# Kernel optimization log

Measured on AMD Instinct MI355X. Metric: run time of the kernel, lower is better.

The kernel has to match this reference:

```python
import jax, jax.numpy as jnp
import numpy as np

ACT_BITS = 8
W_BITS = 8
BN_EPS = 1e-5


def _round_ste(x):
    # straight-through round (HAWQ-style ste_round)
    return x + jax.lax.stop_gradient(jnp.round(x) - x)


def _quant_sym(x, bits):
    # symmetric per-tensor fake quantization; scale treated as constant (EMA min/max in original)
    n = float(2 ** (bits - 1) - 1)
    s = jax.lax.stop_gradient(jnp.maximum(jnp.max(jnp.abs(x)) / n, 1e-8))
    xq = jnp.clip(_round_ste(x / s), -n - 1.0, n) * s
    return xq, s


def _conv(x, w, stride, pad):
    return jax.lax.conv_general_dilated(
        x, w, (stride, stride), [(pad, pad), (pad, pad)],
        dimension_numbers=("NCHW", "OIHW", "NCHW"))


def _quant_bn(x, gamma, beta, mean, var):
    # fold BN into a per-channel scale+bias; quantize the folded scale like a weight
    ws = gamma * jax.lax.rsqrt(var + BN_EPS)          # [C]
    wq, ws_scale = _quant_sym(ws, W_BITS)
    b = beta - mean * wq                               # [C]
    return x * wq[None, :, None, None] + b[None, :, None, None], ws_scale


def setup_inputs() -> dict:
    key = jax.random.key(0)
    ks = jax.random.split(key, 16)
    d = {}
    d["x"] = jax.random.normal(ks[0], (32, 128, 56, 56), jnp.float32)
    d["w1"] = jax.random.normal(ks[1], (256, 128, 3, 3), jnp.float32) * 0.05
    d["w2"] = jax.random.normal(ks[2], (256, 256, 3, 3), jnp.float32) * 0.05
    d["w_id"] = jax.random.normal(ks[3], (256, 128, 1, 1), jnp.float32) * 0.05
    for i, pfx in enumerate(["bn1", "bn2", "id"]):
        k4 = jax.random.split(ks[4 + i], 4)
        d[pfx + "_gamma"] = jax.random.uniform(k4[0], (256,), jnp.float32) + 0.5
        d[pfx + "_beta"] = jax.random.normal(k4[1], (256,), jnp.float32) * 0.1
        d[pfx + "_mean"] = jax.random.normal(k4[2], (256,), jnp.float32) * 0.1
        d[pfx + "_var"] = jax.random.uniform(k4[3], (256,), jnp.float32) + 0.5
    return d


def reference(x, w1, w2, w_id,
              bn1_gamma, bn1_beta, bn1_mean, bn1_var,
              bn2_gamma, bn2_beta, bn2_mean, bn2_var,
              id_gamma, id_beta, id_mean, id_var):
    # quant_act on block input
    xq, act_s = _quant_sym(x, ACT_BITS)

    # identity branch: 1x1 stride-2 quantized conv -> quant_act -> folded quant bn
    w_id_q, _ = _quant_sym(w_id, W_BITS)
    identity = _conv(xq, w_id_q, 2, 0)
    identity, _ = _quant_sym(identity, ACT_BITS)
    identity, _ = _quant_bn(identity, id_gamma, id_beta, id_mean, id_var)

    # main branch conv1 (3x3 stride 2) -> act quant -> bn -> relu -> act quant
    w1_q, _ = _quant_sym(w1, W_BITS)
    h = _conv(xq, w1_q, 2, 1)
    h, _ = _quant_sym(h, ACT_BITS)
    h, _ = _quant_bn(h, bn1_gamma, bn1_beta, bn1_mean, bn1_var)
    h = jax.nn.relu(h)
    h, _ = _quant_sym(h, ACT_BITS)

    # conv2 (3x3 stride 1) -> act quant -> bn
    w2_q, _ = _quant_sym(w2, W_BITS)
    h = _conv(h, w2_q, 1, 1)
    h, _ = _quant_sym(h, ACT_BITS)
    h, _ = _quant_bn(h, bn2_gamma, bn2_beta, bn2_mean, bn2_var)

    # residual add -> int32 requant -> relu
    h = h + identity
    h, out_s = _quant_sym(h, ACT_BITS)
    h = jax.nn.relu(h)
    return h, out_s
```

## Files before the change

kernel.cpp:

```cpp
#include <hip/hip_runtime.h>
#include <limits.h>

#define THREADS 256

typedef int vi4 __attribute__((ext_vector_type(4)));

__device__ __forceinline__ float clamp8f(float q) { return fminf(fmaxf(q, -128.0f), 127.0f); }
__device__ __forceinline__ float sc_from_bits(unsigned b) {
  return fmaxf(__uint_as_float(b) / 127.0f, 1e-8f);
}
__device__ __forceinline__ signed char q8(float v, float s) {
  return (signed char)(int)clamp8f(rintf(v / s));
}


__global__ __launch_bounds__(THREADS) void k_init(int* IS, int* maxv, int* minv) {
  int t = threadIdx.x;
  if (t < 64) IS[t] = 0;
  maxv[t] = INT_MIN;
  minv[t] = INT_MAX;
}

__global__ __launch_bounds__(THREADS) void k_amax(const float4* __restrict__ p, int n4,
                                                  unsigned* __restrict__ slot) {
  const int tid = threadIdx.x;
  const int stride = gridDim.x * THREADS;
  float m = 0.0f;
  int i = blockIdx.x * THREADS + tid;
  for (; i + 3 * stride < n4; i += 4 * stride) {
    float4 v0 = p[i];
    float4 v1 = p[i + stride];
    float4 v2 = p[i + 2 * stride];
    float4 v3 = p[i + 3 * stride];
    float m0 = fmaxf(fmaxf(fabsf(v0.x), fabsf(v0.y)), fmaxf(fabsf(v0.z), fabsf(v0.w)));
    float m1 = fmaxf(fmaxf(fabsf(v1.x), fabsf(v1.y)), fmaxf(fabsf(v1.z), fabsf(v1.w)));
    float m2 = fmaxf(fmaxf(fabsf(v2.x), fabsf(v2.y)), fmaxf(fabsf(v2.z), fabsf(v2.w)));
    float m3 = fmaxf(fmaxf(fabsf(v3.x), fabsf(v3.y)), fmaxf(fabsf(v3.z), fabsf(v3.w)));
    m = fmaxf(m, fmaxf(fmaxf(m0, m1), fmaxf(m2, m3)));
  }
  for (; i < n4; i += stride) {
    float4 v = p[i];
    m = fmaxf(m, fmaxf(fmaxf(fabsf(v.x), fabsf(v.y)), fmaxf(fabsf(v.z), fabsf(v.w))));
  }
#pragma unroll
  for (int k = 32; k >= 1; k >>= 1) m = fmaxf(m, __shfl_xor(m, k));
  __shared__ float wred[4];
  if ((tid & 63) == 0) wred[tid >> 6] = m;
  __syncthreads();
  if (tid == 0) {
    m = fmaxf(fmaxf(wred[0], wred[1]), fmaxf(wred[2], wred[3]));
    atomicMax(slot, __float_as_uint(m));
  }
}

__global__ __launch_bounds__(THREADS) void k_bnfold(const float* __restrict__ gamma,
                                                    const float* __restrict__ beta,
                                                    const float* __restrict__ mean,
                                                    const float* __restrict__ var,
                                                    float* __restrict__ wq, float* __restrict__ bb) {
  __shared__ float red[THREADS];
  int c = threadIdx.x;
  float ws = gamma[c] * (1.0f / sqrtf(var[c] + 1e-5f));
  red[c] = fabsf(ws);
  __syncthreads();
  for (int s = THREADS / 2; s > 0; s >>= 1) {
    if (c < s) red[c] = fmaxf(red[c], red[c + s]);
    __syncthreads();
  }
  float sws = fmaxf(red[0] / 127.0f, 1e-8f);
  float q = clamp8f(rintf(ws / sws)) * sws;
  wq[c] = q;
  bb[c] = beta[c] - mean[c] * q;
}

__global__ __launch_bounds__(THREADS) void k_qx(const float* __restrict__ x, int* __restrict__ X8,
                                                const unsigned* __restrict__ ISu) {
  __shared__ signed char tile[56 * 132];
  float s = sc_from_bits(ISu[0]);
  int b = blockIdx.x;
  int h = b % 56, n = b / 56;
  int t = threadIdx.x;
  const float* xp = x + ((n * 128) * 56 + h) * 56;
#pragma unroll
  for (int k = 0; k < 28; ++k) {
    int i = t + k * 256;
    int w = i % 56, c = i / 56;
    tile[w * 132 + c] = q8(xp[c * 3136 + w], s);
  }
  __syncthreads();
  int* op = X8 + (n * 56 + h) * 56 * 32;
#pragma unroll
  for (int k = 0; k < 7; ++k) {
    int i = t + k * 256;
    int w = i >> 5, c4 = (i & 31) * 4;
    const signed char* tp = tile + w * 132 + c4;
    op[i] = (int)(unsigned char)tp[0] | ((int)(unsigned char)tp[1] << 8) |
            ((int)(unsigned char)tp[2] << 16) | ((int)(unsigned char)tp[3] << 24);
  }
}

__global__ __launch_bounds__(THREADS) void k_qw2m(const float* __restrict__ w, vi4* __restrict__ wm,
                                                  const unsigned* __restrict__ ISu) {
  int t = blockIdx.x * THREADS + threadIdx.x;
  float s = sc_from_bits(ISu[2]);
  int lane = t & 63;
  int cotile = (t >> 6) & 15;
  int ks = t >> 10;
  int tap = ks >> 2, kc = ks & 3;
  int kh = tap / 3, kw = tap % 3;
  int co = cotile * 16 + (lane & 15);
  int ci0 = kc * 64 + (lane >> 4) * 16;
  const float* src = w + (co * 256 + ci0) * 9 + kh * 3 + kw;
  int r[4];
#pragma unroll
  for (int q = 0; q < 4; ++q) {
    unsigned b0 = (unsigned char)q8(src[(q * 4 + 0) * 9], s);
    unsigned b1 = (unsigned char)q8(src[(q * 4 + 1) * 9], s);
    unsigned b2 = (unsigned char)q8(src[(q * 4 + 2) * 9], s);
    unsigned b3 = (unsigned char)q8(src[(q * 4 + 3) * 9], s);
    r[q] = (int)(b0 | (b1 << 8) | (b2 << 16) | (b3 << 24));
  }
  vi4 v = {r[0], r[1], r[2], r[3]};
  wm[t] = v;
}

__global__ __launch_bounds__(THREADS) void k_qw1m(const float* __restrict__ w, vi4* __restrict__ wm,
                                                  const unsigned* __restrict__ ISu) {
  int t = blockIdx.x * THREADS + threadIdx.x;
  float s = sc_from_bits(ISu[1]);
  int lane = t & 63;
  int cotile = (t >> 6) & 15;
  int ks = t >> 10;
  int tap = ks >> 1, kc = ks & 1;
  int kh = tap / 3, kw = tap % 3;
  int co = cotile * 16 + (lane & 15);
  int ci0 = kc * 64 + (lane >> 4) * 16;
  const float* src = w + (co * 128 + ci0) * 9 + kh * 3 + kw;
  int r[4];
#pragma unroll
  for (int q = 0; q < 4; ++q) {
    unsigned b0 = (unsigned char)q8(src[(q * 4 + 0) * 9], s);
    unsigned b1 = (unsigned char)q8(src[(q * 4 + 1) * 9], s);
    unsigned b2 = (unsigned char)q8(src[(q * 4 + 2) * 9], s);
    unsigned b3 = (unsigned char)q8(src[(q * 4 + 3) * 9], s);
    r[q] = (int)(b0 | (b1 << 8) | (b2 << 16) | (b3 << 24));
  }
  vi4 v = {r[0], r[1], r[2], r[3]};
  wm[t] = v;
}

__global__ __launch_bounds__(THREADS) void k_qwidm(const float* __restrict__ w,
                                                   vi4* __restrict__ wm,
                                                   const unsigned* __restrict__ ISu) {
  int t = blockIdx.x * THREADS + threadIdx.x;
  float s = sc_from_bits(ISu[3]);
  int lane = t & 63;
  int cotile = (t >> 6) & 15;
  int ks = t >> 10;
  int co = cotile * 16 + (lane & 15);
  int ci0 = ks * 64 + (lane >> 4) * 16;
  const float* src = w + co * 128 + ci0;
  int r[4];
#pragma unroll
  for (int q = 0; q < 4; ++q) {
    unsigned b0 = (unsigned char)q8(src[q * 4 + 0], s);
    unsigned b1 = (unsigned char)q8(src[q * 4 + 1], s);
    unsigned b2 = (unsigned char)q8(src[q * 4 + 2], s);
    unsigned b3 = (unsigned char)q8(src[q * 4 + 3], s);
    r[q] = (int)(b0 | (b1 << 8) | (b2 << 16) | (b3 << 24));
  }
  vi4 v = {r[0], r[1], r[2], r[3]};
  wm[t] = v;
}

#define MFMA_I8(a, b, c) __builtin_amdgcn_mfma_i32_16x16x64_i8(a, b, c, 0, 0, 0)

__global__ __launch_bounds__(THREADS, 2) void k_conv1(const int* __restrict__ X8,
                                                      const vi4* __restrict__ W1m,
                                                      const vi4* __restrict__ Widm,
                                                      int* __restrict__ H1, int* __restrict__ IDI,
                                                      int* __restrict__ maxS,
                                                      int* __restrict__ minS,
                                                      int* __restrict__ maxabs_id) {
  __shared__ __align__(16) int lds[5 * 58 * 36];
  __shared__ int sMax[2][128], sMin[2][128], redA[4];
  const int tid = threadIdx.x;
  const int bx = blockIdx.x;
  const int n = bx / 28, rr = bx % 28;
  const int hp = rr >> 1, nh = rr & 1;
  const int ho0 = hp * 2;

  for (int r = 0; r < 5; ++r) {
    int h = 2 * ho0 - 1 + r;
    int* dst = lds + r * 58 * 36;
    if (h >= 0 && h < 56) {
      const int* src = X8 + (n * 56 + h) * 56 * 32;
      for (int i = tid; i < 56 * 32; i += THREADS) {
        int col = i >> 5, c = i & 31;
        dst[(col + 1) * 36 + c] = src[i];
      }
      if (tid < 32) dst[tid] = 0;
      else if (tid >= 128 && tid < 160) dst[57 * 36 + (tid - 128)] = 0;
    } else {
      for (int i = tid; i < 58 * 36; i += THREADS) dst[i] = 0;
    }
  }
  __syncthreads();

  const int lane = tid & 63, wv = tid >> 6;
  const int mw = wv & 1, nw = wv >> 1;
  const int lm = lane & 15, quad = lane >> 4;
  const int woc0 = lm, woc1 = (16 + lm) > 27 ? 27 : (16 + lm);
  const int choff = quad * 4;
  const int ho = ho0 + mw;
  const int obase = ((n * 28 + ho) * 28) * 256;
  const int ctbase = nh * 8 + nw * 4;

  vi4 zero = {0, 0, 0, 0};
  vi4 acc[2][4];
  vi4 bcur[4], bnext[4];
  vi4 a0c, a1c, a0n, a1n;

#pragma unroll
  for (int mt = 0; mt < 2; ++mt)
#pragma unroll
    for (int ct = 0; ct < 4; ++ct) acc[mt][ct] = zero;
  const vi4* wibase = Widm + ctbase * 64 + lane;
  {
    const int ro = (2 * mw + 1) * 58;
#pragma unroll
    for (int kc = 0; kc < 2; ++kc) {
      vi4 a0 = *(const vi4*)(lds + (ro + 2 * woc0 + 1) * 36 + kc * 16 + choff);
      vi4 a1 = *(const vi4*)(lds + (ro + 2 * woc1 + 1) * 36 + kc * 16 + choff);
#pragma unroll
      for (int ct = 0; ct < 4; ++ct) {
        vi4 b = wibase[kc * 1024 + ct * 64];
        acc[0][ct] = MFMA_I8(a0, b, acc[0][ct]);
        acc[1][ct] = MFMA_I8(a1, b, acc[1][ct]);
      }
    }
  }
  int am = 0;
#pragma unroll
  for (int ct = 0; ct < 4; ++ct) {
    const int co = (ctbase + ct) * 16 + lm;
#pragma unroll
    for (int mt = 0; mt < 2; ++mt)
#pragma unroll
      for (int r = 0; r < 4; ++r) {
        int wo = mt * 16 + quad * 4 + r;
        if (wo < 28) {
          int v = acc[mt][ct][r];
          IDI[obase + wo * 256 + co] = v;
          am = max(am, v < 0 ? -v : v);
        }
      }
  }
#pragma unroll
  for (int k = 32; k >= 1; k >>= 1) am = max(am, __shfl_xor(am, k));
  if (lane == 0) redA[wv] = am;

#pragma unroll
  for (int mt = 0; mt < 2; ++mt)
#pragma unroll
    for (int ct = 0; ct < 4; ++ct) acc[mt][ct] = zero;
  const vi4* wbase = W1m + ctbase * 64 + lane;
#pragma unroll
  for (int ct = 0; ct < 4; ++ct) bcur[ct] = wbase[ct * 64];
  {
    const int ro = (2 * mw) * 58;
    a0c = *(const vi4*)(lds + (ro + 2 * woc0) * 36 + choff);
    a1c = *(const vi4*)(lds + (ro + 2 * woc1) * 36 + choff);
  }
#pragma unroll 1
  for (int ks = 0; ks < 18; ++ks) {
    int ksn = ks + 1;
    if (ksn < 18) {
      int khn = (ksn >= 6) + (ksn >= 12);
      int t2 = ksn - khn * 6;
      int kwn = t2 >> 1, kcn = t2 & 1;
#pragma unroll
      for (int ct = 0; ct < 4; ++ct) bnext[ct] = wbase[ksn * 1024 + ct * 64];
      int ro = (2 * mw + khn) * 58;
      a0n = *(const vi4*)(lds + (ro + 2 * woc0 + kwn) * 36 + kcn * 16 + choff);
      a1n = *(const vi4*)(lds + (ro + 2 * woc1 + kwn) * 36 + kcn * 16 + choff);
    }
#pragma unroll
    for (int ct = 0; ct < 4; ++ct) {
      acc[0][ct] = MFMA_I8(a0c, bcur[ct], acc[0][ct]);
      acc[1][ct] = MFMA_I8(a1c, bcur[ct], acc[1][ct]);
    }
    a0c = a0n;
    a1c = a1n;
#pragma unroll
    for (int ct = 0; ct < 4; ++ct) bcur[ct] = bnext[ct];
  }

#pragma unroll
  for (int ct = 0; ct < 4; ++ct) {
    const int co = (ctbase + ct) * 16 + lm;
    int vmax = INT_MIN, vmin = INT_MAX;
#pragma unroll
    for (int mt = 0; mt < 2; ++mt)
#pragma unroll
      for (int r = 0; r < 4; ++r) {
        int wo = mt * 16 + quad * 4 + r;
        if (wo < 28) {
          int v = acc[mt][ct][r];
          H1[obase + wo * 256 + co] = v;
          vmax = max(vmax, v);
          vmin = min(vmin, v);
        }
      }
    vmax = max(vmax, __shfl_xor(vmax, 16));
    vmax = max(vmax, __shfl_xor(vmax, 32));
    vmin = min(vmin, __shfl_xor(vmin, 16));
    vmin = min(vmin, __shfl_xor(vmin, 32));
    if (lane < 16) {
      sMax[mw][nw * 64 + ct * 16 + lane] = vmax;
      sMin[mw][nw * 64 + ct * 16 + lane] = vmin;
    }
  }
  __syncthreads();
  if (tid < 128) {
    int row = n * 14 + hp;
    maxS[row * 256 + nh * 128 + tid] = max(sMax[0][tid], sMax[1][tid]);
    minS[row * 256 + nh * 128 + tid] = min(sMin[0][tid], sMin[1][tid]);
  }
  if (tid == 0) {
    int a = max(max(redA[0], redA[1]), max(redA[2], redA[3]));
    atomicMax(maxabs_id, a);
  }
}

__global__ __launch_bounds__(THREADS) void k_red(const int* __restrict__ maxS,
                                                 const int* __restrict__ minS,
                                                 int* __restrict__ maxv, int* __restrict__ minv) {
  int c = threadIdx.x, b = blockIdx.x;
  int vx = INT_MIN, vn = INT_MAX;
#pragma unroll
  for (int r = 0; r < 14; ++r) {
    int row = b * 14 + r;
    vx = max(vx, maxS[row * 256 + c]);
    vn = min(vn, minS[row * 256 + c]);
  }
  atomicMax(&maxv[c], vx);
  atomicMin(&minv[c], vn);
}

__global__ __launch_bounds__(THREADS) void k_s1(int* __restrict__ IS, float* __restrict__ SC,
                                                const int* __restrict__ maxv,
                                                const int* __restrict__ minv,
                                                const float* __restrict__ wq1,
                                                const float* __restrict__ b1) {
  __shared__ int ri[THREADS];
  __shared__ float rf[THREADS];
  int c = threadIdx.x;
  int vmax = maxv[c], vmin = minv[c];
  int a1 = vmax < 0 ? -vmax : vmax;
  int a0 = vmin < 0 ? -vmin : vmin;
  ri[c] = max(a1, a0);
  __syncthreads();
  for (int s = THREADS / 2; s > 0; s >>= 1) {
    if (c < s) ri[c] = max(ri[c], ri[c + s]);
    __syncthreads();
  }
  int mh1 = ri[0];
  const unsigned* ISu = (const unsigned*)IS;
  float sx = sc_from_bits(ISu[0]);
  float sw1 = sc_from_bits(ISu[1]);
  float sxw = sx * sw1;
  float s_h1 = fmaxf(sxw * (float)mh1 / 127.0f, 1e-8f);
  float wq = wq1[c], bbc = b1[c];
  float q1 = clamp8f(rintf((float)vmax * sxw / s_h1));
  float q0 = clamp8f(rintf((float)vmin * sxw / s_h1));
  float hv1 = q1 * s_h1, hv0 = q0 * s_h1;
  float y1 = fmaxf(hv1 * wq + bbc, 0.0f);
  float y0 = fmaxf(hv0 * wq + bbc, 0.0f);
  rf[c] = fmaxf(y1, y0);
  __syncthreads();
  for (int s = THREADS / 2; s > 0; s >>= 1) {
    if (c < s) rf[c] = fmaxf(rf[c], rf[c + s]);
    __syncthreads();
  }
  if (c == 0) {
    IS[4] = mh1;
    SC[7] = rf[0];
    SC[8] = s_h1;
    SC[9] = fmaxf(rf[0] / 127.0f, 1e-8f);
    float swid = sc_from_bits(ISu[3]);
    SC[10] = fmaxf(sx * swid * (float)IS[5] / 127.0f, 1e-8f);
  }
}

__device__ __forceinline__ signed char qact(int v, float sxw, float s_h1, float s_y2, float wq,
                                            float bb) {
  float hf = (float)v * sxw;
  float q = clamp8f(rintf(hf / s_h1));
  float hv = q * s_h1;
  float y = fmaxf(hv * wq + bb, 0.0f);
  float a = fminf(fmaxf(rintf(y / s_y2), -128.0f), 127.0f);
  return (signed char)(int)a;
}

__global__ __launch_bounds__(THREADS) void k_qh1(const int4* __restrict__ H1,
                                                 char4* __restrict__ A2,
                                                 const float* __restrict__ SC,
                                                 const float* __restrict__ wq1,
                                                 const float* __restrict__ b1) {
  int t = blockIdx.x * THREADS + threadIdx.x;
  const unsigned* ISu = (const unsigned*)SC;
  float sx = sc_from_bits(ISu[0]);
  float sw1 = sc_from_bits(ISu[1]);
  float sxw = sx * sw1;
  float s_h1 = SC[8];
  float s_y2 = SC[9];
  int4 v = H1[t];
  int c0 = (t * 4) & 255;
  char4 r;
  r.x = qact(v.x, sxw, s_h1, s_y2, wq1[c0], b1[c0]);
  r.y = qact(v.y, sxw, s_h1, s_y2, wq1[c0 + 1], b1[c0 + 1]);
  r.z = qact(v.z, sxw, s_h1, s_y2, wq1[c0 + 2], b1[c0 + 2]);
  r.w = qact(v.w, sxw, s_h1, s_y2, wq1[c0 + 3], b1[c0 + 3]);
  A2[t] = r;
}

__global__ __launch_bounds__(THREADS, 2) void k_conv2(const int* __restrict__ A2,
                                                      const vi4* __restrict__ W2m,
                                                      int* __restrict__ H2,
                                                      int* __restrict__ maxabs_h2) {
  __shared__ __align__(16) int lds[4 * 30 * 68];
  __shared__ int redA[4];
  const int tid = threadIdx.x;
  const int bx = blockIdx.x;
  const int n = bx / 28, rr = bx % 28;
  const int hp = rr >> 1, nh = rr & 1;
  const int ho0 = hp * 2;

  for (int r = 0; r < 4; ++r) {
    int h = ho0 - 1 + r;
    int* dst = lds + r * 30 * 68;
    if (h >= 0 && h < 28) {
      const int* src = A2 + (n * 28 + h) * 28 * 64;
      for (int i = tid; i < 28 * 64; i += THREADS) {
        int col = i >> 6, c = i & 63;
        dst[(col + 1) * 68 + c] = src[i];
      }
      if (tid < 64) dst[tid] = 0;
      else if (tid >= 128 && tid < 192) dst[29 * 68 + (tid - 128)] = 0;
    } else {
      for (int i = tid; i < 30 * 68; i += THREADS) dst[i] = 0;
    }
  }
  __syncthreads();

  const int lane = tid & 63, wv = tid >> 6;
  const int mw = wv & 1, nw = wv >> 1;
  const int lm = lane & 15, quad = lane >> 4;
  const int woc0 = lm, woc1 = (16 + lm) > 27 ? 27 : (16 + lm);
  const int choff = quad * 4;
  const int ho = ho0 + mw;
  const int ctbase = nh * 8 + nw * 4;

  vi4 zero = {0, 0, 0, 0};
  vi4 acc[2][4];
#pragma unroll
  for (int mt = 0; mt < 2; ++mt)
#pragma unroll
    for (int ct = 0; ct < 4; ++ct) acc[mt][ct] = zero;

  const vi4* wbase = W2m + ctbase * 64 + lane;
  vi4 bcur[4], bnext[4];
  vi4 a0c, a1c, a0n, a1n;
#pragma unroll
  for (int ct = 0; ct < 4; ++ct) bcur[ct] = wbase[ct * 64];
  {
    const int ro = mw * 30;
    a0c = *(const vi4*)(lds + (ro + woc0) * 68 + choff);
    a1c = *(const vi4*)(lds + (ro + woc1) * 68 + choff);
  }
#pragma unroll 1
  for (int ks = 0; ks < 36; ++ks) {
    int ksn = ks + 1;
    if (ksn < 36) {
      int khn = (ksn >= 12) + (ksn >= 24);
      int t2 = ksn - khn * 12;
      int kwn = t2 >> 2, kcn = t2 & 3;
#pragma unroll
      for (int ct = 0; ct < 4; ++ct) bnext[ct] = wbase[ksn * 1024 + ct * 64];
      int ro = (mw + khn) * 30;
      a0n = *(const vi4*)(lds + (ro + woc0 + kwn) * 68 + kcn * 16 + choff);
      a1n = *(const vi4*)(lds + (ro + woc1 + kwn) * 68 + kcn * 16 + choff);
    }
#pragma unroll
    for (int ct = 0; ct < 4; ++ct) {
      acc[0][ct] = MFMA_I8(a0c, bcur[ct], acc[0][ct]);
      acc[1][ct] = MFMA_I8(a1c, bcur[ct], acc[1][ct]);
    }
    a0c = a0n;
    a1c = a1n;
#pragma unroll
    for (int ct = 0; ct < 4; ++ct) bcur[ct] = bnext[ct];
  }

  const int obase = ((n * 28 + ho) * 28) * 256;
  int am = 0;
#pragma unroll
  for (int ct = 0; ct < 4; ++ct) {
    const int co = (ctbase + ct) * 16 + lm;
#pragma unroll
    for (int mt = 0; mt < 2; ++mt)
#pragma unroll
      for (int r = 0; r < 4; ++r) {
        int wo = mt * 16 + quad * 4 + r;
        if (wo < 28) {
          int v = acc[mt][ct][r];
          H2[obase + wo * 256 + co] = v;
          am = max(am, v < 0 ? -v : v);
        }
      }
  }
#pragma unroll
  for (int k = 32; k >= 1; k >>= 1) am = max(am, __shfl_xor(am, k));
  if (lane == 0) redA[wv] = am;
  __syncthreads();
  if (tid == 0) {
    int a = max(max(redA[0], redA[1]), max(redA[2], redA[3]));
    atomicMax(maxabs_h2, a);
  }
}

struct SumParams {
  float sxw2, s_h2, sxwid, s_idq;
};
__device__ __forceinline__ float sum_val(int v2, int vi, const SumParams& P, float wq2c, float b2c,
                                         float wqidc, float bidc) {
  float q2 = clamp8f(rintf((float)v2 * P.sxw2 / P.s_h2));
  float z = (q2 * P.s_h2) * wq2c + b2c;
  float qi = clamp8f(rintf((float)vi * P.sxwid / P.s_idq));
  float zi = (qi * P.s_idq) * wqidc + bidc;
  return z + zi;
}
__device__ __forceinline__ SumParams make_params(const float* SC, const int* IS) {
  const unsigned* ISu = (const unsigned*)IS;
  SumParams P;
  float sx = sc_from_bits(ISu[0]);
  float sw2 = sc_from_bits(ISu[2]);
  float swid = sc_from_bits(ISu[3]);
  float s_y2 = SC[9];
  P.s_idq = SC[10];
  P.sxw2 = s_y2 * sw2;
  P.s_h2 = fmaxf(P.sxw2 * (float)IS[6] / 127.0f, 1e-8f);
  P.sxwid = sx * swid;
  return P;
}

__global__ __launch_bounds__(THREADS) void k_absmax2(const int4* __restrict__ H2,
                                                     const int4* __restrict__ IDI,
                                                     const float* __restrict__ SC,
                                                     const int* __restrict__ IS,
                                                     const float* __restrict__ wq2,
                                                     const float* __restrict__ b2,
                                                     const float* __restrict__ wqid,
                                                     const float* __restrict__ bidp,
                                                     unsigned* __restrict__ slot) {
  __shared__ float pw2[256], pb2[256], pwi[256], pbi[256];
  int tid = threadIdx.x;
  pw2[tid] = wq2[tid];
  pb2[tid] = b2[tid];
  pwi[tid] = wqid[tid];
  pbi[tid] = bidp[tid];
  __syncthreads();
  SumParams P = make_params(SC, IS);
  const int n4 = 1605632;
  const int stride = gridDim.x * THREADS;
  float m = 0.0f;
  for (int i = blockIdx.x * THREADS + tid; i < n4; i += stride) {
    int4 v2 = H2[i];
    int4 vi = IDI[i];
    int c0 = (i * 4) & 255;
    m = fmaxf(m, fabsf(sum_val(v2.x, vi.x, P, pw2[c0], pb2[c0], pwi[c0], pbi[c0])));
    m = fmaxf(m, fabsf(sum_val(v2.y, vi.y, P, pw2[c0 + 1], pb2[c0 + 1], pwi[c0 + 1], pbi[c0 + 1])));
    m = fmaxf(m, fabsf(sum_val(v2.z, vi.z, P, pw2[c0 + 2], pb2[c0 + 2], pwi[c0 + 2], pbi[c0 + 2])));
    m = fmaxf(m, fabsf(sum_val(v2.w, vi.w, P, pw2[c0 + 3], pb2[c0 + 3], pwi[c0 + 3], pbi[c0 + 3])));
  }
#pragma unroll
  for (int k = 32; k >= 1; k >>= 1) m = fmaxf(m, __shfl_xor(m, k));
  __shared__ float wred[4];
  if ((tid & 63) == 0) wred[tid >> 6] = m;
  __syncthreads();
  if (tid == 0) {
    m = fmaxf(fmaxf(wred[0], wred[1]), fmaxf(wred[2], wred[3]));
    atomicMax(slot, __float_as_uint(m));
  }
}

__global__ __launch_bounds__(THREADS) void k_out(const int* __restrict__ H2,
                                                 const int* __restrict__ IDI,
                                                 const float* __restrict__ SC,
                                                 const int* __restrict__ IS,
                                                 const float* __restrict__ wq2,
                                                 const float* __restrict__ b2,
                                                 const float* __restrict__ wqid,
                                                 const float* __restrict__ bidp,
                                                 float* __restrict__ out) {
  __shared__ float tile[64 * 57];
  __shared__ float pw2[64], pb2[64], pwi[64], pbi[64];
  int tid = threadIdx.x;
  int b = blockIdx.x;
  int ct = b & 3;
  int rt = (b >> 2) % 14;
  int n = b / 56;
  int c0 = ct * 64;
  int r0 = rt * 56;
  if (tid < 64) {
    pw2[tid] = wq2[c0 + tid];
    pb2[tid] = b2[c0 + tid];
    pwi[tid] = wqid[c0 + tid];
    pbi[tid] = bidp[c0 + tid];
  }
  __syncthreads();
  SumParams P = make_params(SC, IS);
  float out_s = fmaxf(__uint_as_float(((const unsigned*)IS)[11]) / 127.0f, 1e-8f);

  const int base = (n * 784 + r0) * 256 + c0;
#pragma unroll
  for (int k = 0; k < 14; ++k) {
    int idx = tid + k * 256;
    int rl = idx >> 6;
    int cl = idx & 63;
    int e = base + rl * 256 + cl;
    float sv = sum_val(H2[e], IDI[e], P, pw2[cl], pb2[cl], pwi[cl], pbi[cl]);
    float q = clamp8f(rintf(sv / out_s));
    tile[cl * 57 + rl] = q > 0.0f ? q * out_s : 0.0f;
  }
  __syncthreads();
  float* ob = out + n * 200704 + c0 * 784 + r0;
#pragma unroll
  for (int k = 0; k < 14; ++k) {
    int idx = tid + k * 256;
    int cl = idx / 56;
    int rl = idx % 56;
    ob[cl * 784 + rl] = tile[cl * 57 + rl];
  }
  if (b == 0 && tid == 0) out[6422528] = out_s;
}

extern "C" void kernel_launch(void* const* d_in, const int* in_sizes, int n_in, void* d_out,
                              int out_size, void* d_ws, size_t ws_size, hipStream_t stream) {
  (void)in_sizes; (void)n_in; (void)out_size; (void)ws_size;
  const float* x = (const float*)d_in[0];
  const float* w1 = (const float*)d_in[1];
  const float* w2 = (const float*)d_in[2];
  const float* wid = (const float*)d_in[3];
  const float* bn1g = (const float*)d_in[4];
  const float* bn1b = (const float*)d_in[5];
  const float* bn1m = (const float*)d_in[6];
  const float* bn1v = (const float*)d_in[7];
  const float* bn2g = (const float*)d_in[8];
  const float* bn2b = (const float*)d_in[9];
  const float* bn2m = (const float*)d_in[10];
  const float* bn2v = (const float*)d_in[11];
  const float* idg = (const float*)d_in[12];
  const float* idb = (const float*)d_in[13];
  const float* idm = (const float*)d_in[14];
  const float* idv = (const float*)d_in[15];

  char* ws = (char*)d_ws;
  float* SC = (float*)ws;
  int* IS = (int*)ws;
  unsigned* ISu = (unsigned*)ws;
  int* maxv = (int*)(ws + 1024);
  int* minv = (int*)(ws + 2048);
  float* wq1 = (float*)(ws + 3072);
  float* b1 = (float*)(ws + 4096);
  float* wq2 = (float*)(ws + 5120);
  float* b2 = (float*)(ws + 6144);
  float* wqid = (float*)(ws + 7168);
  float* bid = (float*)(ws + 8192);
  char* X8 = ws + 16384;
  char* A2 = X8;
  char* W1m = X8 + 12845056;
  char* W2m = W1m + 294912;
  char* Widm = W2m + 589824;
  int* H1 = (int*)(Widm + 32768);
  int* H2 = H1;
  int* IDI = (int*)((char*)H1 + 25690112);
  float* out = (float*)d_out;
  int* maxS = (int*)d_out;
  int* minS = maxS + 448 * 256;

  k_init<<<1, THREADS, 0, stream>>>(IS, maxv, minv);
  k_amax<<<512, THREADS, 0, stream>>>((const float4*)x, 3211264, ISu + 0);
  k_amax<<<64, THREADS, 0, stream>>>((const float4*)w1, 73728, ISu + 1);
  k_amax<<<128, THREADS, 0, stream>>>((const float4*)w2, 147456, ISu + 2);
  k_amax<<<16, THREADS, 0, stream>>>((const float4*)wid, 8192, ISu + 3);
  k_bnfold<<<1, THREADS, 0, stream>>>(bn1g, bn1b, bn1m, bn1v, wq1, b1);
  k_bnfold<<<1, THREADS, 0, stream>>>(bn2g, bn2b, bn2m, bn2v, wq2, b2);
  k_bnfold<<<1, THREADS, 0, stream>>>(idg, idb, idm, idv, wqid, bid);
  k_qx<<<1792, THREADS, 0, stream>>>(x, (int*)X8, ISu);
  k_qw1m<<<72, THREADS, 0, stream>>>(w1, (vi4*)W1m, ISu);
  k_qw2m<<<144, THREADS, 0, stream>>>(w2, (vi4*)W2m, ISu);
  k_qwidm<<<8, THREADS, 0, stream>>>(wid, (vi4*)Widm, ISu);
  k_conv1<<<896, THREADS, 0, stream>>>((const int*)X8, (const vi4*)W1m, (const vi4*)Widm, H1, IDI,
                                       maxS, minS, IS + 5);
  k_red<<<32, THREADS, 0, stream>>>(maxS, minS, maxv, minv);
  k_s1<<<1, THREADS, 0, stream>>>(IS, SC, maxv, minv, wq1, b1);
  k_qh1<<<6272, THREADS, 0, stream>>>((const int4*)H1, (char4*)A2, SC, wq1, b1);
  k_conv2<<<896, THREADS, 0, stream>>>((const int*)A2, (const vi4*)W2m, H2, IS + 6);
  k_absmax2<<<1024, THREADS, 0, stream>>>((const int4*)H2, (const int4*)IDI, SC, IS, wq2, b2, wqid,
                                          bid, ISu + 11);
  k_out<<<1792, THREADS, 0, stream>>>(H2, IDI, SC, IS, wq2, b2, wqid, bid, out);
}
```

Measured before the change: 292.9 us.

## Merge preprocessing kernels, vectorize LDS staging loads, fold reduction into scale kernel

The init, absmax and BN-fold kernels are merged into one launch dispatched by block index, and the four quantization kernels into a second launch, with a memset replacing the init kernel. The per-channel min/max reduction and the scale kernel are combined into one single-block kernel that loops over all 448 partial rows. Both conv kernels now stage their input rows into LDS with 16-byte vector loads and stores. Fewer launches cut launch gaps, but the single-block reduction serialises 448 rows of reads on one workgroup.

```diff
diff --git a/kernel.cpp b/kernel.cpp
--- a/kernel.cpp
+++ b/kernel.cpp
@@ -14,19 +14,12 @@
 }
 
 
-__global__ __launch_bounds__(THREADS) void k_init(int* IS, int* maxv, int* minv) {
-  int t = threadIdx.x;
-  if (t < 64) IS[t] = 0;
-  maxv[t] = INT_MIN;
-  minv[t] = INT_MAX;
-}
-
-__global__ __launch_bounds__(THREADS) void k_amax(const float4* __restrict__ p, int n4,
-                                                  unsigned* __restrict__ slot) {
+__device__ __forceinline__ void amax_body(const float4* __restrict__ p, int n4, int bid,
+                                          int nblocks, unsigned* __restrict__ slot) {
   const int tid = threadIdx.x;
-  const int stride = gridDim.x * THREADS;
+  const int stride = nblocks * THREADS;
   float m = 0.0f;
-  int i = blockIdx.x * THREADS + tid;
+  int i = bid * THREADS + tid;
   for (; i + 3 * stride < n4; i += 4 * stride) {
     float4 v0 = p[i];
     float4 v1 = p[i + stride];
@@ -53,124 +46,147 @@
   }
 }
 
-__global__ __launch_bounds__(THREADS) void k_bnfold(const float* __restrict__ gamma,
-                                                    const float* __restrict__ beta,
-                                                    const float* __restrict__ mean,
-                                                    const float* __restrict__ var,
-                                                    float* __restrict__ wq, float* __restrict__ bb) {
-  __shared__ float red[THREADS];
+__global__ __launch_bounds__(THREADS) void k_pre(
+    int* IS, const float* g1, const float* be1, const float* m1, const float* v1, float* wq1,
+    float* b1, const float* g2, const float* be2, const float* m2, const float* v2, float* wq2,
+    float* b2, const float* gi, const float* bei, const float* mi, const float* vvi, float* wqi,
+    float* bi, const float4* w1, const float4* w2, const float4* wid, const float4* x) {
+  unsigned* ISu = (unsigned*)IS;
+  int b = blockIdx.x;
   int c = threadIdx.x;
-  float ws = gamma[c] * (1.0f / sqrtf(var[c] + 1e-5f));
-  red[c] = fabsf(ws);
-  __syncthreads();
-  for (int s = THREADS / 2; s > 0; s >>= 1) {
-    if (c < s) red[c] = fmaxf(red[c], red[c + s]);
+  if (b < 3) {
+    const float *gamma, *beta, *mean, *var;
+    float *wq, *bb;
+    if (b == 0) { gamma = g1; beta = be1; mean = m1; var = v1; wq = wq1; bb = b1; }
+    else if (b == 1) { gamma = g2; beta = be2; mean = m2; var = v2; wq = wq2; bb = b2; }
+    else { gamma = gi; beta = bei; mean = mi; var = vvi; wq = wqi; bb = bi; }
+    __shared__ float red[THREADS];
+    float ws = gamma[c] * (1.0f / sqrtf(var[c] + 1e-5f));
+    red[c] = fabsf(ws);
     __syncthreads();
-  }
-  float sws = fmaxf(red[0] / 127.0f, 1e-8f);
-  float q = clamp8f(rintf(ws / sws)) * sws;
-  wq[c] = q;
-  bb[c] = beta[c] - mean[c] * q;
-}
-
-__global__ __launch_bounds__(THREADS) void k_qx(const float* __restrict__ x, int* __restrict__ X8,
-                                                const unsigned* __restrict__ ISu) {
+    for (int s = THREADS / 2; s > 0; s >>= 1) {
+      if (c < s) red[c] = fmaxf(red[c], red[c + s]);
+      __syncthreads();
+    }
+    float sws = fmaxf(red[0] / 127.0f, 1e-8f);
+    float q = clamp8f(rintf(ws / sws)) * sws;
+    wq[c] = q;
+    bb[c] = beta[c] - mean[c] * q;
+    return;
+  }
+  b -= 3;
+  if (b < 64) { amax_body(w1, 73728, b, 64, ISu + 1); return; }
+  b -= 64;
+  if (b < 128) { amax_body(w2, 147456, b, 128, ISu + 2); return; }
+  b -= 128;
+  if (b < 16) { amax_body(wid, 8192, b, 16, ISu + 3); return; }
+  b -= 16;
+  amax_body(x, 3211264, b, 512, ISu + 0);
+}
+
+__global__ __launch_bounds__(THREADS) void k_quant(const float* __restrict__ x,
+                                                   int* __restrict__ X8,
+                                                   const float* __restrict__ w1f,
+                                                   vi4* __restrict__ W1m,
+                                                   const float* __restrict__ w2f,
+                                                   vi4* __restrict__ W2m,
+                                                   const float* __restrict__ widf,
+                                                   vi4* __restrict__ Widm,
+                                                   const unsigned* __restrict__ ISu) {
   __shared__ signed char tile[56 * 132];
-  float s = sc_from_bits(ISu[0]);
   int b = blockIdx.x;
-  int h = b % 56, n = b / 56;
   int t = threadIdx.x;
-  const float* xp = x + ((n * 128) * 56 + h) * 56;
-#pragma unroll
-  for (int k = 0; k < 28; ++k) {
-    int i = t + k * 256;
-    int w = i % 56, c = i / 56;
-    tile[w * 132 + c] = q8(xp[c * 3136 + w], s);
-  }
-  __syncthreads();
-  int* op = X8 + (n * 56 + h) * 56 * 32;
-#pragma unroll
-  for (int k = 0; k < 7; ++k) {
-    int i = t + k * 256;
-    int w = i >> 5, c4 = (i & 31) * 4;
-    const signed char* tp = tile + w * 132 + c4;
-    op[i] = (int)(unsigned char)tp[0] | ((int)(unsigned char)tp[1] << 8) |
-            ((int)(unsigned char)tp[2] << 16) | ((int)(unsigned char)tp[3] << 24);
-  }
-}
-
-__global__ __launch_bounds__(THREADS) void k_qw2m(const float* __restrict__ w, vi4* __restrict__ wm,
-                                                  const unsigned* __restrict__ ISu) {
-  int t = blockIdx.x * THREADS + threadIdx.x;
-  float s = sc_from_bits(ISu[2]);
-  int lane = t & 63;
-  int cotile = (t >> 6) & 15;
-  int ks = t >> 10;
-  int tap = ks >> 2, kc = ks & 3;
-  int kh = tap / 3, kw = tap % 3;
-  int co = cotile * 16 + (lane & 15);
-  int ci0 = kc * 64 + (lane >> 4) * 16;
-  const float* src = w + (co * 256 + ci0) * 9 + kh * 3 + kw;
-  int r[4];
-#pragma unroll
-  for (int q = 0; q < 4; ++q) {
-    unsigned b0 = (unsigned char)q8(src[(q * 4 + 0) * 9], s);
-    unsigned b1 = (unsigned char)q8(src[(q * 4 + 1) * 9], s);
-    unsigned b2 = (unsigned char)q8(src[(q * 4 + 2) * 9], s);
-    unsigned b3 = (unsigned char)q8(src[(q * 4 + 3) * 9], s);
-    r[q] = (int)(b0 | (b1 << 8) | (b2 << 16) | (b3 << 24));
-  }
-  vi4 v = {r[0], r[1], r[2], r[3]};
-  wm[t] = v;
-}
-
-__global__ __launch_bounds__(THREADS) void k_qw1m(const float* __restrict__ w, vi4* __restrict__ wm,
-                                                  const unsigned* __restrict__ ISu) {
-  int t = blockIdx.x * THREADS + threadIdx.x;
-  float s = sc_from_bits(ISu[1]);
-  int lane = t & 63;
-  int cotile = (t >> 6) & 15;
-  int ks = t >> 10;
-  int tap = ks >> 1, kc = ks & 1;
-  int kh = tap / 3, kw = tap % 3;
-  int co = cotile * 16 + (lane & 15);
-  int ci0 = kc * 64 + (lane >> 4) * 16;
-  const float* src = w + (co * 128 + ci0) * 9 + kh * 3 + kw;
-  int r[4];
-#pragma unroll
-  for (int q = 0; q < 4; ++q) {
-    unsigned b0 = (unsigned char)q8(src[(q * 4 + 0) * 9], s);
-    unsigned b1 = (unsigned char)q8(src[(q * 4 + 1) * 9], s);
-    unsigned b2 = (unsigned char)q8(src[(q * 4 + 2) * 9], s);
-    unsigned b3 = (unsigned char)q8(src[(q * 4 + 3) * 9], s);
-    r[q] = (int)(b0 | (b1 << 8) | (b2 << 16) | (b3 << 24));
-  }
-  vi4 v = {r[0], r[1], r[2], r[3]};
-  wm[t] = v;
-}
-
-__global__ __launch_bounds__(THREADS) void k_qwidm(const float* __restrict__ w,
-                                                   vi4* __restrict__ wm,
-                                                   const unsigned* __restrict__ ISu) {
-  int t = blockIdx.x * THREADS + threadIdx.x;
-  float s = sc_from_bits(ISu[3]);
-  int lane = t & 63;
-  int cotile = (t >> 6) & 15;
-  int ks = t >> 10;
-  int co = cotile * 16 + (lane & 15);
-  int ci0 = ks * 64 + (lane >> 4) * 16;
-  const float* src = w + co * 128 + ci0;
-  int r[4];
-#pragma unroll
-  for (int q = 0; q < 4; ++q) {
-    unsigned b0 = (unsigned char)q8(src[q * 4 + 0], s);
-    unsigned b1 = (unsigned char)q8(src[q * 4 + 1], s);
-    unsigned b2 = (unsigned char)q8(src[q * 4 + 2], s);
-    unsigned b3 = (unsigned char)q8(src[q * 4 + 3], s);
-    r[q] = (int)(b0 | (b1 << 8) | (b2 << 16) | (b3 << 24));
-  }
-  vi4 v = {r[0], r[1], r[2], r[3]};
-  wm[t] = v;
+  if (b < 1792) {
+    float s = sc_from_bits(ISu[0]);
+    int h = b % 56, n = b / 56;
+    const float* xp = x + ((n * 128) * 56 + h) * 56;
+#pragma unroll
+    for (int k = 0; k < 28; ++k) {
+      int i = t + k * 256;
+      int w = i % 56, c = i / 56;
+      tile[w * 132 + c] = q8(xp[c * 3136 + w], s);
+    }
+    __syncthreads();
+    int* op = X8 + (n * 56 + h) * 56 * 32;
+#pragma unroll
+    for (int k = 0; k < 7; ++k) {
+      int i = t + k * 256;
+      int w = i >> 5, c4 = (i & 31) * 4;
+      const signed char* tp = tile + w * 132 + c4;
+      op[i] = (int)(unsigned char)tp[0] | ((int)(unsigned char)tp[1] << 8) |
+              ((int)(unsigned char)tp[2] << 16) | ((int)(unsigned char)tp[3] << 24);
+    }
+    return;
+  }
+  if (b < 1864) {
+    int tt = (b - 1792) * THREADS + t;
+    float s = sc_from_bits(ISu[1]);
+    int lane = tt & 63;
+    int cotile = (tt >> 6) & 15;
+    int ks = tt >> 10;
+    int tap = ks >> 1, kc = ks & 1;
+    int kh = tap / 3, kw = tap % 3;
+    int co = cotile * 16 + (lane & 15);
+    int ci0 = kc * 64 + (lane >> 4) * 16;
+    const float* src = w1f + (co * 128 + ci0) * 9 + kh * 3 + kw;
+    int r[4];
+#pragma unroll
+    for (int q = 0; q < 4; ++q) {
+      unsigned b0 = (unsigned char)q8(src[(q * 4 + 0) * 9], s);
+      unsigned b1 = (unsigned char)q8(src[(q * 4 + 1) * 9], s);
+      unsigned b2 = (unsigned char)q8(src[(q * 4 + 2) * 9], s);
+      unsigned b3 = (unsigned char)q8(src[(q * 4 + 3) * 9], s);
+      r[q] = (int)(b0 | (b1 << 8) | (b2 << 16) | (b3 << 24));
+    }
+    vi4 v = {r[0], r[1], r[2], r[3]};
+    W1m[tt] = v;
+    return;
+  }
+  if (b < 2008) {
+    int tt = (b - 1864) * THREADS + t;
+    float s = sc_from_bits(ISu[2]);
+    int lane = tt & 63;
+    int cotile = (tt >> 6) & 15;
+    int ks = tt >> 10;
+    int tap = ks >> 2, kc = ks & 3;
+    int kh = tap / 3, kw = tap % 3;
+    int co = cotile * 16 + (lane & 15);
+    int ci0 = kc * 64 + (lane >> 4) * 16;
+    const float* src = w2f + (co * 256 + ci0) * 9 + kh * 3 + kw;
+    int r[4];
+#pragma unroll
+    for (int q = 0; q < 4; ++q) {
+      unsigned b0 = (unsigned char)q8(src[(q * 4 + 0) * 9], s);
+      unsigned b1 = (unsigned char)q8(src[(q * 4 + 1) * 9], s);
+      unsigned b2 = (unsigned char)q8(src[(q * 4 + 2) * 9], s);
+      unsigned b3 = (unsigned char)q8(src[(q * 4 + 3) * 9], s);
+      r[q] = (int)(b0 | (b1 << 8) | (b2 << 16) | (b3 << 24));
+    }
+    vi4 v = {r[0], r[1], r[2], r[3]};
+    W2m[tt] = v;
+    return;
+  }
+  {
+    int tt = (b - 2008) * THREADS + t;
+    float s = sc_from_bits(ISu[3]);
+    int lane = tt & 63;
+    int cotile = (tt >> 6) & 15;
+    int ks = tt >> 10;
+    int co = cotile * 16 + (lane & 15);
+    int ci0 = ks * 64 + (lane >> 4) * 16;
+    const float* src = widf + co * 128 + ci0;
+    int r[4];
+#pragma unroll
+    for (int q = 0; q < 4; ++q) {
+      unsigned b0 = (unsigned char)q8(src[q * 4 + 0], s);
+      unsigned b1 = (unsigned char)q8(src[q * 4 + 1], s);
+      unsigned b2 = (unsigned char)q8(src[q * 4 + 2], s);
+      unsigned b3 = (unsigned char)q8(src[q * 4 + 3], s);
+      r[q] = (int)(b0 | (b1 << 8) | (b2 << 16) | (b3 << 24));
+    }
+    vi4 v = {r[0], r[1], r[2], r[3]};
+    Widm[tt] = v;
+  }
 }
 
 #define MFMA_I8(a, b, c) __builtin_amdgcn_mfma_i32_16x16x64_i8(a, b, c, 0, 0, 0)
@@ -189,20 +205,21 @@
   const int n = bx / 28, rr = bx % 28;
   const int hp = rr >> 1, nh = rr & 1;
   const int ho0 = hp * 2;
+  vi4 zero = {0, 0, 0, 0};
 
   for (int r = 0; r < 5; ++r) {
     int h = 2 * ho0 - 1 + r;
     int* dst = lds + r * 58 * 36;
     if (h >= 0 && h < 56) {
-      const int* src = X8 + (n * 56 + h) * 56 * 32;
-      for (int i = tid; i < 56 * 32; i += THREADS) {
-        int col = i >> 5, c = i & 31;
-        dst[(col + 1) * 36 + c] = src[i];
+      const vi4* src = (const vi4*)(X8 + (n * 56 + h) * 56 * 32);
+      for (int i4 = tid; i4 < 448; i4 += THREADS) {
+        int col = i4 >> 3, c = (i4 & 7) * 4;
+        *(vi4*)(dst + (col + 1) * 36 + c) = src[i4];
       }
       if (tid < 32) dst[tid] = 0;
       else if (tid >= 128 && tid < 160) dst[57 * 36 + (tid - 128)] = 0;
     } else {
-      for (int i = tid; i < 58 * 36; i += THREADS) dst[i] = 0;
+      for (int i4 = tid; i4 < 522; i4 += THREADS) ((vi4*)dst)[i4] = zero;
     }
   }
   __syncthreads();
@@ -216,7 +233,6 @@
   const int obase = ((n * 28 + ho) * 28) * 256;
   const int ctbase = nh * 8 + nw * 4;
 
-  vi4 zero = {0, 0, 0, 0};
   vi4 acc[2][4];
   vi4 bcur[4], bnext[4];
   vi4 a0c, a1c, a0n, a1n;
@@ -333,30 +349,20 @@
   }
 }
 
-__global__ __launch_bounds__(THREADS) void k_red(const int* __restrict__ maxS,
+__global__ __launch_bounds__(THREADS) void k_rs1(int* __restrict__ IS, float* __restrict__ SC,
+                                                 const int* __restrict__ maxS,
                                                  const int* __restrict__ minS,
-                                                 int* __restrict__ maxv, int* __restrict__ minv) {
-  int c = threadIdx.x, b = blockIdx.x;
-  int vx = INT_MIN, vn = INT_MAX;
-#pragma unroll
-  for (int r = 0; r < 14; ++r) {
-    int row = b * 14 + r;
-    vx = max(vx, maxS[row * 256 + c]);
-    vn = min(vn, minS[row * 256 + c]);
-  }
-  atomicMax(&maxv[c], vx);
-  atomicMin(&minv[c], vn);
-}
-
-__global__ __launch_bounds__(THREADS) void k_s1(int* __restrict__ IS, float* __restrict__ SC,
-                                                const int* __restrict__ maxv,
-                                                const int* __restrict__ minv,
-                                                const float* __restrict__ wq1,
-                                                const float* __restrict__ b1) {
+                                                 const float* __restrict__ wq1,
+                                                 const float* __restrict__ b1) {
   __shared__ int ri[THREADS];
   __shared__ float rf[THREADS];
   int c = threadIdx.x;
-  int vmax = maxv[c], vmin = minv[c];
+  int vmax = INT_MIN, vmin = INT_MAX;
+#pragma unroll 4
+  for (int r = 0; r < 448; ++r) {
+    vmax = max(vmax, maxS[r * 256 + c]);
+    vmin = min(vmin, minS[r * 256 + c]);
+  }
   int a1 = vmax < 0 ? -vmax : vmax;
   int a0 = vmin < 0 ? -vmin : vmin;
   ri[c] = max(a1, a0);
@@ -436,20 +442,21 @@
   const int n = bx / 28, rr = bx % 28;
   const int hp = rr >> 1, nh = rr & 1;
   const int ho0 = hp * 2;
+  vi4 zero = {0, 0, 0, 0};
 
   for (int r = 0; r < 4; ++r) {
     int h = ho0 - 1 + r;
     int* dst = lds + r * 30 * 68;
     if (h >= 0 && h < 28) {
-      const int* src = A2 + (n * 28 + h) * 28 * 64;
-      for (int i = tid; i < 28 * 64; i += THREADS) {
-        int col = i >> 6, c = i & 63;
-        dst[(col + 1) * 68 + c] = src[i];
+      const vi4* src = (const vi4*)(A2 + (n * 28 + h) * 28 * 64);
+      for (int i4 = tid; i4 < 448; i4 += THREADS) {
+        int col = i4 >> 4, c = (i4 & 15) * 4;
+        *(vi4*)(dst + (col + 1) * 68 + c) = src[i4];
       }
       if (tid < 64) dst[tid] = 0;
       else if (tid >= 128 && tid < 192) dst[29 * 68 + (tid - 128)] = 0;
     } else {
-      for (int i = tid; i < 30 * 68; i += THREADS) dst[i] = 0;
+      for (int i4 = tid; i4 < 510; i4 += THREADS) ((vi4*)dst)[i4] = zero;
     }
   }
   __syncthreads();
@@ -462,16 +469,15 @@
   const int ho = ho0 + mw;
   const int ctbase = nh * 8 + nw * 4;
 
-  vi4 zero = {0, 0, 0, 0};
   vi4 acc[2][4];
-#pragma unroll
-  for (int mt = 0; mt < 2; ++mt)
-#pragma unroll
-    for (int ct = 0; ct < 4; ++ct) acc[mt][ct] = zero;
-
-  const vi4* wbase = W2m + ctbase * 64 + lane;
   vi4 bcur[4], bnext[4];
   vi4 a0c, a1c, a0n, a1n;
+#pragma unroll
+  for (int mt = 0; mt < 2; ++mt)
+#pragma unroll
+    for (int ct = 0; ct < 4; ++ct) acc[mt][ct] = zero;
+
+  const vi4* wbase = W2m + ctbase * 64 + lane;
 #pragma unroll
   for (int ct = 0; ct < 4; ++ct) bcur[ct] = wbase[ct * 64];
   {
@@ -670,8 +676,6 @@
   float* SC = (float*)ws;
   int* IS = (int*)ws;
   unsigned* ISu = (unsigned*)ws;
-  int* maxv = (int*)(ws + 1024);
-  int* minv = (int*)(ws + 2048);
   float* wq1 = (float*)(ws + 3072);
   float* b1 = (float*)(ws + 4096);
   float* wq2 = (float*)(ws + 5120);
@@ -690,22 +694,15 @@
   int* maxS = (int*)d_out;
   int* minS = maxS + 448 * 256;
 
-  k_init<<<1, THREADS, 0, stream>>>(IS, maxv, minv);
-  k_amax<<<512, THREADS, 0, stream>>>((const float4*)x, 3211264, ISu + 0);
-  k_amax<<<64, THREADS, 0, stream>>>((const float4*)w1, 73728, ISu + 1);
-  k_amax<<<128, THREADS, 0, stream>>>((const float4*)w2, 147456, ISu + 2);
-  k_amax<<<16, THREADS, 0, stream>>>((const float4*)wid, 8192, ISu + 3);
-  k_bnfold<<<1, THREADS, 0, stream>>>(bn1g, bn1b, bn1m, bn1v, wq1, b1);
-  k_bnfold<<<1, THREADS, 0, stream>>>(bn2g, bn2b, bn2m, bn2v, wq2, b2);
-  k_bnfold<<<1, THREADS, 0, stream>>>(idg, idb, idm, idv, wqid, bid);
-  k_qx<<<1792, THREADS, 0, stream>>>(x, (int*)X8, ISu);
-  k_qw1m<<<72, THREADS, 0, stream>>>(w1, (vi4*)W1m, ISu);
-  k_qw2m<<<144, THREADS, 0, stream>>>(w2, (vi4*)W2m, ISu);
-  k_qwidm<<<8, THREADS, 0, stream>>>(wid, (vi4*)Widm, ISu);
+  hipMemsetAsync(IS, 0, 256, stream);
+  k_pre<<<723, THREADS, 0, stream>>>(IS, bn1g, bn1b, bn1m, bn1v, wq1, b1, bn2g, bn2b, bn2m, bn2v,
+                                     wq2, b2, idg, idb, idm, idv, wqid, bid, (const float4*)w1,
+                                     (const float4*)w2, (const float4*)wid, (const float4*)x);
+  k_quant<<<2016, THREADS, 0, stream>>>(x, (int*)X8, w1, (vi4*)W1m, w2, (vi4*)W2m, wid,
+                                        (vi4*)Widm, ISu);
   k_conv1<<<896, THREADS, 0, stream>>>((const int*)X8, (const vi4*)W1m, (const vi4*)Widm, H1, IDI,
                                        maxS, minS, IS + 5);
-  k_red<<<32, THREADS, 0, stream>>>(maxS, minS, maxv, minv);
-  k_s1<<<1, THREADS, 0, stream>>>(IS, SC, maxv, minv, wq1, b1);
+  k_rs1<<<1, THREADS, 0, stream>>>(IS, SC, maxS, minS, wq1, b1);
   k_qh1<<<6272, THREADS, 0, stream>>>((const int4*)H1, (char4*)A2, SC, wq1, b1);
   k_conv2<<<896, THREADS, 0, stream>>>((const int*)A2, (const vi4*)W2m, H2, IS + 6);
   k_absmax2<<<1024, THREADS, 0, stream>>>((const int4*)H2, (const int4*)IDI, SC, IS, wq2, b2, wqid,
```

Measured after the change: 271.2 us. -7.4%, faster.
